# Optimization experiments

Hardware: AMD Instinct MI355X
Metric: run time of the kernel (lower is better)

## Reference

```python
import jax, jax.numpy as jnp
import numpy as np

B, N, K = 2, 8192, 9
FEAT_C, COST_C, FLOW_C = 128, 64, 3
CH = [128, 128]          # PointConv output channels
MLP = [128, 64]          # pointwise Conv1d channels
WN = 16                  # WeightNet output width
HID = [8, 8]             # WeightNet hidden widths
SLOPE = 0.1              # leaky relu slope
EPS = 1e-5
CLAMP = (-200.0, 200.0)


def setup_inputs() -> dict:
    key = jax.random.key(0)
    ks = iter(jax.random.split(key, 64))
    def nrm(shape, s=0.02):
        return jax.random.normal(next(ks), shape, jnp.float32) * s
    inp = {}
    inp["xyz"] = jax.random.normal(next(ks), (B, N, 3), jnp.float32)
    inp["feats"] = jax.random.normal(next(ks), (B, FEAT_C, N), jnp.float32)
    inp["cost_volume"] = jax.random.normal(next(ks), (B, COST_C, N), jnp.float32)
    inp["flow"] = jax.random.normal(next(ks), (B, FLOW_C, N), jnp.float32)
    last = FEAT_C + COST_C + FLOW_C
    for i, co in enumerate(CH):
        cin = last + 3
        p = f"pc{i}_"
        inp[p + "w1"] = nrm((HID[0], 3)); inp[p + "b1"] = jnp.zeros((HID[0],), jnp.float32)
        inp[p + "w2"] = nrm((HID[1], HID[0])); inp[p + "b2"] = jnp.zeros((HID[1],), jnp.float32)
        inp[p + "w3"] = nrm((WN, HID[1])); inp[p + "b3"] = jnp.zeros((WN,), jnp.float32)
        inp[p + "linW"] = nrm((co, cin * WN)); inp[p + "linb"] = jnp.zeros((co,), jnp.float32)
        last = co
    for i, co in enumerate(MLP):
        inp[f"mlp{i}_W"] = nrm((co, last)); inp[f"mlp{i}_b"] = jnp.zeros((co,), jnp.float32)
        last = co
    inp["fc_W"] = nrm((3, last)); inp["fc_b"] = jnp.zeros((3,), jnp.float32)
    return inp


def _bn(x, axes):
    m = x.mean(axes, keepdims=True)
    v = x.var(axes, keepdims=True)
    return (x - m) / jnp.sqrt(v + EPS)


def _leaky(x):
    return jnp.where(x >= 0, x, SLOPE * x)


def _knn_idx(xyz, k):
    # xyz: [B,N,3] -> idx [B,N,K] of k nearest (incl. self)
    sq = jnp.sum(xyz * xyz, -1)                       # [B,N]
    d = sq[:, :, None] + sq[:, None, :] - 2.0 * jnp.einsum('bnc,bmc->bnm', xyz, xyz)
    return jax.lax.top_k(-d, k)[1]                    # [B,N,K]


def _gather(a, idx):
    # a: [B,N,C], idx: [B,N,K] -> [B,N,K,C]
    return jax.vmap(lambda x, i: x[i])(a, idx)


def _pointconv(xyz, points, idx, w1, b1, w2, b2, w3, b3, linW, linb):
    # xyz [B,N,3], points [B,C,N] -> [B,out,N]
    g_xyz = _gather(xyz, idx) - xyz[:, :, None, :]    # [B,N,K,3] relative coords
    g_pts = _gather(jnp.transpose(points, (0, 2, 1)), idx)  # [B,N,K,C]
    grouped = jnp.concatenate([g_pts, g_xyz], -1)     # [B,N,K,C+3]
    # WeightNet on relative coords: 3 -> 8 -> 8 -> 16 (bn+relu each)
    h = jax.nn.relu(_bn(g_xyz @ w1.T + b1, (0, 1, 2)))
    h = jax.nn.relu(_bn(h @ w2.T + b2, (0, 1, 2)))
    w = jax.nn.relu(_bn(h @ w3.T + b3, (0, 1, 2)))    # [B,N,K,WN]
    bsz, n = grouped.shape[0], grouped.shape[1]
    agg = jnp.einsum('bnkc,bnkw->bncw', grouped, w).reshape(bsz, n, -1)
    out = agg @ linW.T + linb                         # [B,N,out]
    out = _leaky(_bn(out, (0, 1)))
    return jnp.transpose(out, (0, 2, 1))              # [B,out,N]


def reference(xyz, feats, cost_volume, flow,
              pc0_w1, pc0_b1, pc0_w2, pc0_b2, pc0_w3, pc0_b3, pc0_linW, pc0_linb,
              pc1_w1, pc1_b1, pc1_w2, pc1_b2, pc1_w3, pc1_b3, pc1_linW, pc1_linb,
              mlp0_W, mlp0_b, mlp1_W, mlp1_b, fc_W, fc_b):
    idx = _knn_idx(xyz, K)
    x = jnp.concatenate([feats, cost_volume, flow], axis=1)  # [B, feat+cost+flow, N]
    x = _pointconv(xyz, x, idx, pc0_w1, pc0_b1, pc0_w2, pc0_b2, pc0_w3, pc0_b3, pc0_linW, pc0_linb)
    x = _pointconv(xyz, x, idx, pc1_w1, pc1_b1, pc1_w2, pc1_b2, pc1_w3, pc1_b3, pc1_linW, pc1_linb)
    x = _leaky(jnp.einsum('oc,bcn->bon', mlp0_W, x) + mlp0_b[None, :, None])
    x = _leaky(jnp.einsum('oc,bcn->bon', mlp1_W, x) + mlp1_b[None, :, None])
    fl = jnp.einsum('oc,bcn->bon', fc_W, x) + fc_b[None, :, None]
    return x, jnp.clip(fl, CLAMP[0], CLAMP[1])
```

## Files before the change

kernel.cpp:

```cpp
#include <hip/hip_runtime.h>

#define NBATCH 2
#define NPTS   8192
#define NPT    (NBATCH*NPTS)
#define KNN    9
#define SEG    16
#define SEGN   (NPTS/SEG)
#define SCAP   16
#define SSTR   17

typedef unsigned short u16;
typedef unsigned int   u32;
typedef short bf16x8 __attribute__((ext_vector_type(8)));
typedef float f32x4  __attribute__((ext_vector_type(4)));

__device__ __forceinline__ float wred(float v){
#pragma unroll
  for(int o=32;o>0;o>>=1) v += __shfl_down(v,o);
  return v;
}

__device__ __forceinline__ u16 f2b(float f){
  u32 u = __float_as_uint(f);
  return (u16)((u + 0x7fffu + ((u>>16)&1u)) >> 16);
}

__device__ __forceinline__ float bumpup(float x){
  u32 u = __float_as_uint(x);
  if(u == 0x80000000u) u = 1u;
  else if((int)u >= 0) u += 1u;
  else u -= 1u;
  return __uint_as_float(u);
}

__global__ __launch_bounds__(256) void k_build_xin(
    const float* __restrict__ feats, const float* __restrict__ cost,
    const float* __restrict__ flow, float* __restrict__ xin)
{
  __shared__ float buf[196][67];
  int t = threadIdx.x;
  int pt0 = blockIdx.x*64;
  int b = pt0 >> 13, n0 = pt0 & (NPTS-1);
  int lane = t & 63, grp = t >> 6;
  const float* f  = feats + (size_t)b*128*NPTS + n0 + lane;
  const float* cv = cost  + (size_t)b*64 *NPTS + n0 + lane;
  const float* fl = flow  + (size_t)b*3  *NPTS + n0 + lane;
  for(int c=grp; c<128; c+=4) buf[c][lane]      = f[(size_t)c*NPTS];
  for(int c=grp; c<64;  c+=4) buf[128+c][lane]  = cv[(size_t)c*NPTS];
  if(grp<3) buf[192+grp][lane] = fl[(size_t)grp*NPTS];
  else      buf[195][lane] = 0.f;
  __syncthreads();
  for(int e=t; e<64*49; e+=256){
    int p = e/49, q = e-p*49;
    float4 v = make_float4(buf[4*q][p], buf[4*q+1][p], buf[4*q+2][p], buf[4*q+3][p]);
    *(float4*)(xin + (size_t)(pt0+p)*196 + 4*q) = v;
  }
}

__global__ __launch_bounds__(256) void k_thr(
    const float* __restrict__ xyz, float* __restrict__ thr)
{
  __shared__ float md[4][64][9];
  int t = threadIdx.x, lane = t & 63, wave = t >> 6;
  int qb = blockIdx.x;
  int b = qb >> 7;
  int n = (qb & 127)*64 + lane;
  const float* xb = xyz + (size_t)b*NPTS*3;
  float qx=xb[3*n], qy=xb[3*n+1], qz=xb[3*n+2];
  float qs = __fadd_rn(__fadd_rn(__fmul_rn(qx,qx),__fmul_rn(qy,qy)),__fmul_rn(qz,qz));
  float bd[KNN];
#pragma unroll
  for(int i=0;i<KNN;i++) bd[i]=__builtin_inff();
  for(int i=0;i<128;i++){
    int m = (wave*128 + i)*16;
    float cx=xb[3*m], cy=xb[3*m+1], cz=xb[3*m+2];
    float s = __fadd_rn(__fadd_rn(__fmul_rn(cx,cx),__fmul_rn(cy,cy)),__fmul_rn(cz,cz));
    float dot = fmaf(cz,qz, fmaf(cy,qy, __fmul_rn(cx,qx)));
    float d = __fsub_rn(__fadd_rn(qs,s), __fmul_rn(2.0f,dot));
    if(d < bd[KNN-1]){
      bd[KNN-1]=d;
#pragma unroll
      for(int r=KNN-2;r>=0;r--){
        if(bd[r+1] < bd[r]){ float td=bd[r]; bd[r]=bd[r+1]; bd[r+1]=td; }
      }
    }
  }
#pragma unroll
  for(int i=0;i<KNN;i++) md[wave][lane][i]=bd[i];
  __syncthreads();
  if(t < 64){
    float b2[KNN];
#pragma unroll
    for(int i=0;i<KNN;i++) b2[i]=__builtin_inff();
    for(int w=0;w<4;w++){
#pragma unroll
      for(int i=0;i<KNN;i++){
        float d = md[w][t][i];
        if(d < b2[KNN-1]){
          b2[KNN-1]=d;
#pragma unroll
          for(int r=KNN-2;r>=0;r--){
            if(b2[r+1] < b2[r]){ float td=b2[r]; b2[r]=b2[r+1]; b2[r+1]=td; }
          }
        }
      }
    }
    thr[(b<<13) + (qb & 127)*64 + t] = b2[KNN-1];
  }
}

__global__ __launch_bounds__(256) void k_knn_part(
    const float* __restrict__ xyz, const float* __restrict__ thr,
    float* __restrict__ pd, int* __restrict__ pi)
{
  __shared__ float4 cbuf[256];
  __shared__ float sdq[256*SSTR];
  __shared__ int   sqi[256*SSTR];
  int t = threadIdx.x;
  int seg = blockIdx.x & (SEG-1);
  int qc  = blockIdx.x >> 4;
  int b = qc >> 5;
  int n = (qc & 31)*256 + t;
  int pt = (b<<13) + n;
  const float* xb = xyz + (size_t)b*NPTS*3;
  float qx=xb[3*n], qy=xb[3*n+1], qz=xb[3*n+2];
  float qs = __fadd_rn(__fadd_rn(__fmul_rn(qx,qx),__fmul_rn(qy,qy)),__fmul_rn(qz,qz));
  float init = bumpup(thr[pt]);
  float bd[KNN]; int bi[KNN];
#pragma unroll
  for(int i=0;i<KNN;i++){ bd[i]=init; bi[i]=0x7fffffff; }
  float cut = init;
  int cnt = 0;
  float* msd = sdq + t*SSTR;
  int*   msi = sqi + t*SSTR;
  auto flush = [&](){
    for(int i=0;i<cnt;i++){
      float d = msd[i]; int id = msi[i];
      if(d < bd[KNN-1]){
        bd[KNN-1]=d; bi[KNN-1]=id;
#pragma unroll
        for(int r=KNN-2;r>=0;r--){
          if(bd[r+1] < bd[r]){
            float td=bd[r]; bd[r]=bd[r+1]; bd[r+1]=td;
            int ti=bi[r]; bi[r]=bi[r+1]; bi[r+1]=ti;
          }
        }
      }
    }
    cnt = 0;
    cut = bd[KNN-1];
  };
  const int m0 = seg*SEGN;
  for(int tt=0; tt<SEGN; tt+=256){
    int m = m0 + tt + t;
    float cx=xb[3*m], cy=xb[3*m+1], cz=xb[3*m+2];
    float s = __fadd_rn(__fadd_rn(__fmul_rn(cx,cx),__fmul_rn(cy,cy)),__fmul_rn(cz,cz));
    cbuf[t] = make_float4(cx,cy,cz,s);
    __syncthreads();
    for(int j0=0; j0<256; j0+=8){
      float dv[8];
#pragma unroll
      for(int u=0;u<8;u++){
        float4 c = cbuf[j0+u];
        float dot = fmaf(c.z,qz, fmaf(c.y,qy, __fmul_rn(c.x,qx)));
        dv[u] = __fsub_rn(__fadd_rn(qs,c.w), __fmul_rn(2.0f,dot));
      }
#pragma unroll
      for(int u=0;u<8;u++){
        if(dv[u] < cut){
          msd[cnt]=dv[u]; msi[cnt]=m0+tt+j0+u; cnt++;
          if(cnt==SCAP) flush();
        }
      }
    }
    __syncthreads();
  }
  flush();
  size_t base = ((size_t)pt*SEG + seg)*KNN;
#pragma unroll
  for(int i=0;i<KNN;i++){ pd[base+i]=bd[i]; pi[base+i]=bi[i]; }
}

__global__ __launch_bounds__(256) void k_knn_merge(
    const float* __restrict__ pd, const int* __restrict__ pi, int* __restrict__ idxo)
{
  int pt = blockIdx.x*256 + threadIdx.x;
  const float4* dp = (const float4*)(pd + (size_t)pt*SEG*KNN);
  const int4*   ip = (const int4*)(pi + (size_t)pt*SEG*KNN);
  float bd[KNN]; int bi[KNN];
#pragma unroll
  for(int i=0;i<KNN;i++){ bd[i]=__builtin_inff(); bi[i]=0x7fffffff; }
  for(int v=0; v<SEG*KNN/4; v++){
    float4 dv = dp[v];
    int4   iv = ip[v];
    float dd[4] = {dv.x,dv.y,dv.z,dv.w};
    int   ii[4] = {iv.x,iv.y,iv.z,iv.w};
#pragma unroll
    for(int u=0;u<4;u++){
      float d = dd[u]; int id = ii[u];
      if(d < bd[KNN-1]){
        bd[KNN-1]=d; bi[KNN-1]=id;
#pragma unroll
        for(int i=KNN-2;i>=0;i--){
          if(bd[i+1] < bd[i]){
            float td=bd[i]; bd[i]=bd[i+1]; bd[i+1]=td;
            int ti=bi[i]; bi[i]=bi[i+1]; bi[i+1]=ti;
          }
        }
      }
    }
  }
#pragma unroll
  for(int r=0;r<KNN;r++) idxo[pt*KNN + r] = bi[r];
}

__global__ __launch_bounds__(256) void k_wn1(
    const float* __restrict__ xyz, const int* __restrict__ idx,
    const float* __restrict__ W, const float* __restrict__ Bv,
    float* __restrict__ hout, float* __restrict__ partial)
{
  int t = threadIdx.x;
  int e = blockIdx.x*256 + t;
  int pt = e/KNN;
  int b = pt>>13, n = pt & (NPTS-1);
  int m = idx[e];
  const float* xb = xyz + (size_t)b*NPTS*3;
  float gx = xb[3*m]-xb[3*n], gy = xb[3*m+1]-xb[3*n+1], gz = xb[3*m+2]-xb[3*n+2];
  float v[8];
#pragma unroll
  for(int j=0;j<8;j++){
    float d = fmaf(gz, W[3*j+2], fmaf(gy, W[3*j+1], gx*W[3*j]));
    v[j] = d + Bv[j];
    hout[(size_t)e*8 + j] = v[j];
  }
  __shared__ float red[4][2][8];
  int wave = t>>6, lane = t&63;
#pragma unroll
  for(int j=0;j<8;j++){
    float s = wred(v[j]);
    float q = wred(v[j]*v[j]);
    if(lane==0){ red[wave][0][j]=s; red[wave][1][j]=q; }
  }
  __syncthreads();
  if(t < 16){
    int isq = t>>3, c = t&7;
    partial[blockIdx.x*16 + t] =
      red[0][isq][c]+red[1][isq][c]+red[2][isq][c]+red[3][isq][c];
  }
}

template<int CI, int CO>
__global__ __launch_bounds__(256) void k_wn23(
    const float* __restrict__ hin, const float* __restrict__ partialIn,
    int nb, float cnt,
    const float* __restrict__ W, const float* __restrict__ Bv,
    float* __restrict__ hout, float* __restrict__ partialOut)
{
  __shared__ float sa[256], qa[256];
  __shared__ float stl[2*CI];
  int t = threadIdx.x;
  {
    int c = t % CI;
    int r0 = t / CI;
    int stride = 256 / CI;
    float s=0.f, q=0.f;
    for(int r=r0; r<nb; r+=stride){
      s += partialIn[r*2*CI + c];
      q += partialIn[r*2*CI + CI + c];
    }
    sa[t]=s; qa[t]=q;
    __syncthreads();
    if(t < CI){
      for(int g=1; g<stride; g++){ s += sa[t+g*CI]; q += qa[t+g*CI]; }
      float mean = s/cnt;
      float var  = q/cnt - mean*mean;
      stl[t]    = mean;
      stl[CI+t] = 1.0f/sqrtf(var + 1e-5f);
    }
    __syncthreads();
  }
  int e = blockIdx.x*256 + t;
  float x[CI];
#pragma unroll
  for(int i=0;i<CI;i++){
    float v = (hin[(size_t)e*CI + i] - stl[i])*stl[CI+i];
    x[i] = v>0.f? v : 0.f;
  }
  float v[CO];
#pragma unroll
  for(int j=0;j<CO;j++){
    float d = 0.f;
#pragma unroll
    for(int i=0;i<CI;i++) d = fmaf(x[i], W[j*CI+i], d);
    v[j] = d + Bv[j];
    hout[(size_t)e*CO + j] = v[j];
  }
  __shared__ float red[4][2][CO];
  int wave = t>>6, lane = t&63;
#pragma unroll
  for(int j=0;j<CO;j++){
    float s = wred(v[j]);
    float q = wred(v[j]*v[j]);
    if(lane==0){ red[wave][0][j]=s; red[wave][1][j]=q; }
  }
  __syncthreads();
  if(t < 2*CO){
    int isq = t/CO, c = t%CO;
    partialOut[blockIdx.x*2*CO + t] =
      red[0][isq][c]+red[1][isq][c]+red[2][isq][c]+red[3][isq][c];
  }
}

__global__ __launch_bounds__(256) void k_fin(
    const float* __restrict__ partial, float* __restrict__ st,
    int C, int nb, float cnt)
{
  __shared__ float sa[256], qa[256];
  int t = threadIdx.x;
  int c = t % C;
  int r0 = t / C;
  int stride = 256 / C;
  float s=0.f, q=0.f;
  for(int r=r0; r<nb; r+=stride){
    s += partial[r*2*C + c];
    q += partial[r*2*C + C + c];
  }
  sa[t]=s; qa[t]=q;
  __syncthreads();
  if(t < C){
    for(int g=1; g<stride; g++){ s += sa[t+g*C]; q += qa[t+g*C]; }
    float mean = s/cnt;
    float var  = q/cnt - mean*mean;
    st[t]   = mean;
    st[C+t] = 1.0f/sqrtf(var + 1e-5f);
  }
}

__global__ __launch_bounds__(256) void k_prepW(
    const float* __restrict__ linW, u16* __restrict__ Wh, int AW, int KP)
{
  int e = blockIdx.x*256 + threadIdx.x;
  if(e >= 128*KP) return;
  int o = e / KP, k = e - o*KP;
  float w = (k < AW) ? linW[o*AW + k] : 0.f;
  Wh[e] = f2b(w);
}

template<int CIN, int XSTRIDE, int KP>
__global__ __launch_bounds__(256) void k_buildA(
    const float* __restrict__ xin, const float* __restrict__ xyz,
    const int* __restrict__ idx, const float* __restrict__ wpre,
    const float* __restrict__ st3, u16* __restrict__ Abuf, int c0)
{
  constexpr int P = 16;
  constexpr int CPTS = CIN-3;
  constexpr int CPAD = KP/16;
  __shared__ float wm[P][KNN][16];
  __shared__ float gxs[P][KNN][3];
  __shared__ int   si[P][KNN];
  __shared__ float sm3[16], sr3[16];
  int t = threadIdx.x;
  int pt0 = c0 + blockIdx.x*P;
  int b = pt0 >> 13;
  const float* xb = xyz + (size_t)b*NPTS*3;
  if(t<16){ sm3[t]=st3[t]; sr3[t]=st3[16+t]; }
  for(int e=t; e<P*KNN; e+=256){
    int p = e/KNN, k = e - p*KNN;
    int n = (pt0+p)&(NPTS-1);
    int m = idx[(pt0+p)*KNN+k];
    si[p][k]=m;
    gxs[p][k][0]=xb[3*m]  -xb[3*n];
    gxs[p][k][1]=xb[3*m+1]-xb[3*n+1];
    gxs[p][k][2]=xb[3*m+2]-xb[3*n+2];
  }
  __syncthreads();
  for(int e=t; e<P*KNN*16; e+=256){
    int p = e/(KNN*16); int r = e - p*(KNN*16); int k = r>>4, wn = r&15;
    float v = (wpre[((size_t)(pt0+p)*KNN + k)*16 + wn] - sm3[wn]) * sr3[wn];
    wm[p][k][wn] = v>0.f? v:0.f;
  }
  __syncthreads();
  for(int it=t; it<P*CPAD; it+=256){
    int p = it/CPAD, c = it - p*CPAD;
    u32 u[8];
    if(c < CIN){
      float g[KNN];
      if(c < CPTS){
#pragma unroll
        for(int k=0;k<KNN;k++)
          g[k] = xin[(size_t)((b<<13) + si[p][k])*XSTRIDE + c];
      } else {
        int cc = c - CPTS;
#pragma unroll
        for(int k=0;k<KNN;k++) g[k] = gxs[p][k][cc];
      }
      float a[16];
#pragma unroll
      for(int wn=0; wn<16; wn++){
        float s = 0.f;
#pragma unroll
        for(int k=0;k<KNN;k++) s = fmaf(g[k], wm[p][k][wn], s);
        a[wn] = s;
      }
#pragma unroll
      for(int j=0;j<8;j++)
        u[j] = (u32)f2b(a[2*j]) | ((u32)f2b(a[2*j+1])<<16);
    } else {
#pragma unroll
      for(int j=0;j<8;j++) u[j]=0;
    }
    u32* dst = (u32*)(Abuf + ((size_t)(blockIdx.x*P + p)*KP + c*16));
    uint4 v0 = make_uint4(u[0],u[1],u[2],u[3]);
    uint4 v1 = make_uint4(u[4],u[5],u[6],u[7]);
    *(uint4*)dst = v0;
    *((uint4*)dst + 1) = v1;
  }
}

__device__ __forceinline__ void gload16(const void* g, void* l){
  __builtin_amdgcn_global_load_lds(
      (const __attribute__((address_space(1))) u32*)g,
      (__attribute__((address_space(3))) u32*)l, 16, 0, 0);
}

template<int KP>
__global__ __launch_bounds__(512) void k_gemm(
    const u16* __restrict__ Wh, const u16* __restrict__ A,
    const float* __restrict__ linb, float* __restrict__ outp,
    float* __restrict__ partial, int ptBase)
{
  __shared__ __attribute__((aligned(16))) u16 lds[24576];
  constexpr int NT = KP/64;
  int t = threadIdx.x, wave = t>>6, lane = t&63;
  int p0 = blockIdx.x*64;
  const u16* Ab = A + (size_t)p0*KP;

  auto stage = [&](const u16* __restrict__ g, int k0, int ldsByteOff, int rows){
    int nr = (rows*128) >> 13;
    for(int r=0;r<nr;r++){
      int y  = (r*8 + wave) << 10;
      int yl = y + lane*16;
      int row = yl >> 7;
      int s = (yl >> 4) & 7;
      int c = s ^ (row & 7);
      const u16* src = g + (size_t)row*KP + k0 + c*8;
      gload16(src, (char*)lds + ldsByteOff + y);
    }
  };

  stage(Wh, 0, 0,     128);
  stage(Ab, 0, 32768, 64);

  f32x4 acc[4];
#pragma unroll
  for(int j=0;j<4;j++) acc[j]=(f32x4)(0.f);

  for(int kt=0; kt<NT; kt++){
    int cur = kt & 1;
    __syncthreads();
    if(kt+1 < NT){
      int nxt = cur^1;
      stage(Wh, (kt+1)*64, nxt*16384,         128);
      stage(Ab, (kt+1)*64, 32768 + nxt*8192,  64);
    }
    const u16* Lw = lds + cur*8192;
    const u16* La = lds + 16384 + cur*4096;
#pragma unroll
    for(int kf=0; kf<2; kf++){
      int cb = kf*4 + (lane>>4);
      bf16x8 af[4];
#pragma unroll
      for(int nf=0; nf<4; nf++){
        int p = nf*16 + (lane&15);
        af[nf] = *(const bf16x8*)(La + p*64 + ((cb ^ (p&7))<<3));
      }
      int row = wave*16 + (lane&15);
      bf16x8 wh = *(const bf16x8*)(Lw + row*64 + ((cb ^ (row&7))<<3));
#pragma unroll
      for(int nf=0; nf<4; nf++)
        acc[nf] = __builtin_amdgcn_mfma_f32_16x16x32_bf16(wh, af[nf], acc[nf], 0,0,0);
    }
  }

  int gb = (ptBase>>6) + blockIdx.x;
  int q = lane>>4, lc = lane&15;
  int obase = wave*16 + q*4;
#pragma unroll
  for(int r=0;r<4;r++){
    int o = obase + r;
    float bo = linb[o];
    float sv = 0.f, qv = 0.f;
#pragma unroll
    for(int nf=0; nf<4; nf++){
      float x = acc[nf][r] + bo;
      outp[(size_t)(ptBase + p0 + nf*16 + lc)*128 + o] = x;
      sv += x; qv = fmaf(x,x,qv);
    }
#pragma unroll
    for(int off=8; off>0; off>>=1){
      sv += __shfl_down(sv,off);
      qv += __shfl_down(qv,off);
    }
    if(lc==0){
      partial[gb*256 + o]       = sv;
      partial[gb*256 + 128 + o] = qv;
    }
  }
}

__global__ __launch_bounds__(256) void k_pfin(
    const float* __restrict__ outp, const float* __restrict__ st,
    float* __restrict__ xout)
{
  int e = blockIdx.x*256 + threadIdx.x;
  int c = e & 127;
  float v = (outp[e]-st[c])*st[128+c];
  xout[e] = v>=0.f? v : 0.1f*v;
}

__global__ __launch_bounds__(512) void k_mlp(
    const float* __restrict__ x2,
    const float* __restrict__ W0, const float* __restrict__ B0,
    const float* __restrict__ W1, const float* __restrict__ B1,
    const float* __restrict__ Wf, const float* __restrict__ Bf,
    float* __restrict__ dout)
{
  __shared__ float w0l[128*129];
  __shared__ float w1l[128*65];
  __shared__ float xt [128*65];
  __shared__ float m1l[64*65];
  int t = threadIdx.x;
  int pt0 = blockIdx.x*64;
  int b = pt0 >> 13, n0 = pt0 & (NPTS-1);
  for(int e=t; e<128*128; e+=512){ int o=e>>7, j=e&127; w0l[j*129+o] = W0[e]; }
  for(int e=t; e<64*128;  e+=512){ int o=e>>7, j=e&127; w1l[j*65+o]  = W1[e]; }
  for(int e=t; e<64*128;  e+=512){ int p=e>>7, j=e&127; xt[j*65+p]   = x2[(size_t)(pt0+p)*128 + j]; }
  __syncthreads();
  int p = t&63, wv = t>>6;
  float acc[16];
#pragma unroll
  for(int i=0;i<16;i++) acc[i]=0.f;
  for(int j=0;j<128;j++){
    float xv = xt[j*65+p];
#pragma unroll
    for(int i=0;i<16;i++)
      acc[i] = fmaf(w0l[j*129 + wv*16 + i], xv, acc[i]);
  }
  __syncthreads();
#pragma unroll
  for(int i=0;i<16;i++){
    int o = wv*16+i;
    float v = acc[i] + B0[o];
    v = v>=0.f? v : 0.1f*v;
    xt[o*65 + p] = v;
  }
  __syncthreads();
  float a2[8];
#pragma unroll
  for(int i=0;i<8;i++) a2[i]=0.f;
  for(int j=0;j<128;j++){
    float xv = xt[j*65+p];
#pragma unroll
    for(int i=0;i<8;i++)
      a2[i] = fmaf(w1l[j*65 + wv*8 + i], xv, a2[i]);
  }
#pragma unroll
  for(int i=0;i<8;i++){
    int o = wv*8+i;
    float v = a2[i] + B1[o];
    v = v>=0.f? v : 0.1f*v;
    dout[(size_t)(b*64+o)*NPTS + n0 + p] = v;
    m1l[o*65+p] = v;
  }
  __syncthreads();
  if(t < 192){
    int o = t/64, pp = t%64;
    float a = Bf[o];
    for(int j=0;j<64;j++) a = fmaf(Wf[o*64+j], m1l[j*65+pp], a);
    a = fminf(fmaxf(a, -200.f), 200.f);
    dout[(size_t)NBATCH*64*NPTS + (size_t)(b*3+o)*NPTS + n0 + pp] = a;
  }
}

extern "C" void kernel_launch(void* const* d_in, const int* in_sizes, int n_in,
                              void* d_out, int out_size, void* d_ws, size_t ws_size,
                              hipStream_t stream)
{
  (void)in_sizes; (void)n_in; (void)out_size;
  const float* xyz   = (const float*)d_in[0];
  const float* feats = (const float*)d_in[1];
  const float* cost  = (const float*)d_in[2];
  const float* flow  = (const float*)d_in[3];
  const float* pw1[2]  = {(const float*)d_in[4],  (const float*)d_in[12]};
  const float* pb1[2]  = {(const float*)d_in[5],  (const float*)d_in[13]};
  const float* pw2[2]  = {(const float*)d_in[6],  (const float*)d_in[14]};
  const float* pb2[2]  = {(const float*)d_in[7],  (const float*)d_in[15]};
  const float* pw3[2]  = {(const float*)d_in[8],  (const float*)d_in[16]};
  const float* pb3[2]  = {(const float*)d_in[9],  (const float*)d_in[17]};
  const float* plW[2]  = {(const float*)d_in[10], (const float*)d_in[18]};
  const float* plb[2]  = {(const float*)d_in[11], (const float*)d_in[19]};
  const float* m0W = (const float*)d_in[20];
  const float* m0b = (const float*)d_in[21];
  const float* m1W = (const float*)d_in[22];
  const float* m1b = (const float*)d_in[23];
  const float* fcW = (const float*)d_in[24];
  const float* fcb = (const float*)d_in[25];
  float* out = (float*)d_out;

  const int KP0 = 3200, AW0 = 3168;
  const int KP1 = 2112, AW1 = 2096;

  float* ws = (float*)d_ws;
  size_t o = 0;
  float* xin0 = ws + o; o += (size_t)NPT*196;
  int*   idx  = (int*)(ws + o); o += (size_t)NPT*KNN + 3;
  o &= ~(size_t)3;
  float* thr  = ws + o; o += (size_t)NPT;
  float* pd   = ws + o; o += (size_t)NPT*SEG*KNN;
  int*   pi   = (int*)(ws + o); o += (size_t)NPT*SEG*KNN;
  float* h1   = ws + o; o += (size_t)NPT*KNN*8;
  float* h2   = ws + o; o += (size_t)NPT*KNN*8;
  float* wpre = ws + o; o += (size_t)NPT*KNN*16;
  float* part1 = ws + o; o += 576*16;
  float* part2 = ws + o; o += 576*16;
  float* part3 = ws + o; o += 576*32;
  float* parto = ws + o; o += 65536;
  float* st3  = ws + o; o += 32;
  float* sto  = ws + o; o += 256;
  float* outp = ws + o; o += (size_t)NPT*128;
  float* x1   = ws + o; o += (size_t)NPT*128;
  float* x2   = ws + o; o += (size_t)NPT*128;
  u16* Wh0 = (u16*)(ws + o); o += (size_t)128*KP0/2;
  u16* Wh1 = (u16*)(ws + o); o += (size_t)128*KP1/2;
  u16* Abuf = (u16*)(ws + o);
  size_t used_bytes = o*4;
  size_t avail = ws_size > used_bytes ? ws_size - used_bytes : 0;
  int npc = NPT;
  while(npc > 1024 && (size_t)npc*KP0*2 > avail) npc >>= 1;

  k_build_xin<<<NPT/64, 256, 0, stream>>>(feats, cost, flow, xin0);
  k_thr<<<256, 256, 0, stream>>>(xyz, thr);
  k_knn_part<<<64*SEG, 256, 0, stream>>>(xyz, thr, pd, pi);
  k_knn_merge<<<NPT/256, 256, 0, stream>>>(pd, pi, idx);

  k_prepW<<<(128*KP0+255)/256, 256, 0, stream>>>(plW[0], Wh0, AW0, KP0);
  k_prepW<<<(128*KP1+255)/256, 256, 0, stream>>>(plW[1], Wh1, AW1, KP1);

  const float cnt1 = (float)(NPT*KNN);
  const float cnto = (float)NPT;

  for(int L=0; L<2; ++L){
    k_wn1<<<576,256,0,stream>>>(xyz, idx, pw1[L], pb1[L], h1, part1);
    k_wn23<8,8><<<576,256,0,stream>>>(h1, part1, 576, cnt1, pw2[L], pb2[L], h2, part2);
    k_wn23<8,16><<<576,256,0,stream>>>(h2, part2, 576, cnt1, pw3[L], pb3[L], wpre, part3);
    k_fin<<<1,256,0,stream>>>(part3, st3, 16, 576, cnt1);
    for(int c0 = 0; c0 < NPT; c0 += npc){
      if(L==0){
        k_buildA<198,196,KP0><<<npc/16,256,0,stream>>>(xin0, xyz, idx, wpre, st3, Abuf, c0);
        k_gemm<KP0><<<npc/64,512,0,stream>>>(Wh0, Abuf, plb[0], outp, parto, c0);
      } else {
        k_buildA<131,128,KP1><<<npc/16,256,0,stream>>>(x1, xyz, idx, wpre, st3, Abuf, c0);
        k_gemm<KP1><<<npc/64,512,0,stream>>>(Wh1, Abuf, plb[1], outp, parto, c0);
      }
    }
    k_fin<<<1,256,0,stream>>>(parto, sto, 128, NPT/64, cnto);
    k_pfin<<<NPT*128/256,256,0,stream>>>(outp, sto, (L==0)? x1 : x2);
  }

  k_mlp<<<NPT/64,512,0,stream>>>(x2, m0W,m0b, m1W,m1b, fcW,fcb, out);
}
```

Before: 561.2 us.

## Fuse BN/leaky epilogues into consumers, derive WeightNet layer-1 stats from xyz moments

Removes the k_pfin pass by applying the PointConv batch-norm and leaky ReLU inside the next buildA gather and inside k_mlp's load. WeightNet layer-1 BN statistics are now computed analytically from first and second moments of neighbour offsets, accumulated once in k_knn_merge, so the k_wn1 kernel and its h1 buffer are dropped and layer 1 is fused into the layer-2 kernel. The knn candidate insertion becomes branchless, always writing to the scratch slot and flushing when more than 8 are pending. Costs are repeated BN work on gathered neighbours (9x redundant) and a small serial reduction at the start of every wn23a block.

New measurement: 566.4 us. No clear change (+0.9%).

```diff
diff --git a/kernel.cpp b/kernel.cpp
--- a/kernel.cpp
+++ b/kernel.cpp
@@ -121,7 +121,8 @@
   int qc  = blockIdx.x >> 4;
   int b = qc >> 5;
   int n = (qc & 31)*256 + t;
-  int pt = (b<<13) + n;
+  int pt = (b<<13) + t + (qc&31)*256;
+  pt = (b<<13) + n;
   const float* xb = xyz + (size_t)b*NPTS*3;
   float qx=xb[3*n], qy=xb[3*n+1], qz=xb[3*n+2];
   float qs = __fadd_rn(__fadd_rn(__fmul_rn(qx,qx),__fmul_rn(qy,qy)),__fmul_rn(qz,qz));
@@ -167,11 +168,11 @@
       }
 #pragma unroll
       for(int u=0;u<8;u++){
-        if(dv[u] < cut){
-          msd[cnt]=dv[u]; msi[cnt]=m0+tt+j0+u; cnt++;
-          if(cnt==SCAP) flush();
-        }
-      }
+        msd[cnt] = dv[u];
+        msi[cnt] = m0+tt+j0+u;
+        cnt += (dv[u] < cut) ? 1 : 0;
+      }
+      if(cnt > 8) flush();
     }
     __syncthreads();
   }
@@ -182,9 +183,15 @@
 }
 
 __global__ __launch_bounds__(256) void k_knn_merge(
-    const float* __restrict__ pd, const int* __restrict__ pi, int* __restrict__ idxo)
-{
-  int pt = blockIdx.x*256 + threadIdx.x;
+    const float* __restrict__ xyz,
+    const float* __restrict__ pd, const int* __restrict__ pi,
+    int* __restrict__ idxo, float* __restrict__ gpart)
+{
+  __shared__ float red[4][9];
+  int t = threadIdx.x;
+  int pt = blockIdx.x*256 + t;
+  int b = pt >> 13, n = pt & (NPTS-1);
+  const float* xb = xyz + (size_t)b*NPTS*3;
   const float4* dp = (const float4*)(pd + (size_t)pt*SEG*KNN);
   const int4*   ip = (const int4*)(pi + (size_t)pt*SEG*KNN);
   float bd[KNN]; int bi[KNN];
@@ -212,25 +219,82 @@
   }
 #pragma unroll
   for(int r=0;r<KNN;r++) idxo[pt*KNN + r] = bi[r];
-}
-
-__global__ __launch_bounds__(256) void k_wn1(
+  float q0=xb[3*n], q1=xb[3*n+1], q2=xb[3*n+2];
+  float mom[9];
+#pragma unroll
+  for(int i=0;i<9;i++) mom[i]=0.f;
+#pragma unroll
+  for(int r=0;r<KNN;r++){
+    int m = bi[r];
+    float gx=xb[3*m]-q0, gy=xb[3*m+1]-q1, gz=xb[3*m+2]-q2;
+    mom[0]+=gx; mom[1]+=gy; mom[2]+=gz;
+    mom[3]=fmaf(gx,gx,mom[3]); mom[4]=fmaf(gy,gy,mom[4]); mom[5]=fmaf(gz,gz,mom[5]);
+    mom[6]=fmaf(gx,gy,mom[6]); mom[7]=fmaf(gx,gz,mom[7]); mom[8]=fmaf(gy,gz,mom[8]);
+  }
+  int wave = t>>6, lane = t&63;
+#pragma unroll
+  for(int i=0;i<9;i++){
+    float s = wred(mom[i]);
+    if(lane==0) red[wave][i]=s;
+  }
+  __syncthreads();
+  if(t<9)
+    gpart[blockIdx.x*9 + t] = red[0][t]+red[1][t]+red[2][t]+red[3][t];
+}
+
+__global__ __launch_bounds__(256) void k_wn23a(
     const float* __restrict__ xyz, const int* __restrict__ idx,
-    const float* __restrict__ W, const float* __restrict__ Bv,
-    float* __restrict__ hout, float* __restrict__ partial)
-{
+    const float* __restrict__ gpart, float cnt,
+    const float* __restrict__ W1, const float* __restrict__ B1,
+    const float* __restrict__ W2, const float* __restrict__ B2,
+    float* __restrict__ hout, float* __restrict__ partialOut)
+{
+  __shared__ float mom[9];
+  __shared__ float stl[16];
   int t = threadIdx.x;
+  if(t<9){
+    float s=0.f;
+    for(int r=0;r<64;r++) s += gpart[r*9+t];
+    mom[t]=s;
+  }
+  __syncthreads();
+  if(t<8){
+    float inv = 1.0f/cnt;
+    float w0=W1[3*t], w1=W1[3*t+1], w2=W1[3*t+2], bb=B1[t];
+    float Eg0=mom[0]*inv, Eg1=mom[1]*inv, Eg2=mom[2]*inv;
+    float Mxx=mom[3]*inv, Myy=mom[4]*inv, Mzz=mom[5]*inv;
+    float Mxy=mom[6]*inv, Mxz=mom[7]*inv, Myz=mom[8]*inv;
+    float mu_lin = w0*Eg0 + w1*Eg1 + w2*Eg2;
+    float mean = mu_lin + bb;
+    float e2 = w0*w0*Mxx + w1*w1*Myy + w2*w2*Mzz
+             + 2.f*(w0*w1*Mxy + w0*w2*Mxz + w1*w2*Myz)
+             + 2.f*bb*mu_lin + bb*bb;
+    float var = e2 - mean*mean;
+    stl[t] = mean;
+    stl[8+t] = 1.0f/sqrtf(var + 1e-5f);
+  }
+  __syncthreads();
   int e = blockIdx.x*256 + t;
   int pt = e/KNN;
   int b = pt>>13, n = pt & (NPTS-1);
   int m = idx[e];
   const float* xb = xyz + (size_t)b*NPTS*3;
   float gx = xb[3*m]-xb[3*n], gy = xb[3*m+1]-xb[3*n+1], gz = xb[3*m+2]-xb[3*n+2];
+  float x[8];
+#pragma unroll
+  for(int j=0;j<8;j++){
+    float d = fmaf(gz, W1[3*j+2], fmaf(gy, W1[3*j+1], gx*W1[3*j]));
+    float v = d + B1[j];
+    v = (v - stl[j])*stl[8+j];
+    x[j] = v>0.f? v : 0.f;
+  }
   float v[8];
 #pragma unroll
   for(int j=0;j<8;j++){
-    float d = fmaf(gz, W[3*j+2], fmaf(gy, W[3*j+1], gx*W[3*j]));
-    v[j] = d + Bv[j];
+    float d = 0.f;
+#pragma unroll
+    for(int i=0;i<8;i++) d = fmaf(x[i], W2[j*8+i], d);
+    v[j] = d + B2[j];
     hout[(size_t)e*8 + j] = v[j];
   }
   __shared__ float red[4][2][8];
@@ -244,7 +308,7 @@
   __syncthreads();
   if(t < 16){
     int isq = t>>3, c = t&7;
-    partial[blockIdx.x*16 + t] =
+    partialOut[blockIdx.x*16 + t] =
       red[0][isq][c]+red[1][isq][c]+red[2][isq][c]+red[3][isq][c];
   }
 }
@@ -346,11 +410,12 @@
   Wh[e] = f2b(w);
 }
 
-template<int CIN, int XSTRIDE, int KP>
+template<int CIN, int XSTRIDE, int KP, bool BN>
 __global__ __launch_bounds__(256) void k_buildA(
     const float* __restrict__ xin, const float* __restrict__ xyz,
     const int* __restrict__ idx, const float* __restrict__ wpre,
-    const float* __restrict__ st3, u16* __restrict__ Abuf, int c0)
+    const float* __restrict__ st3, const float* __restrict__ bnst,
+    u16* __restrict__ Abuf, int c0)
 {
   constexpr int P = 16;
   constexpr int CPTS = CIN-3;
@@ -389,6 +454,14 @@
 #pragma unroll
         for(int k=0;k<KNN;k++)
           g[k] = xin[(size_t)((b<<13) + si[p][k])*XSTRIDE + c];
+        if(BN){
+          float sm = bnst[c], sr = bnst[128+c];
+#pragma unroll
+          for(int k=0;k<KNN;k++){
+            float v = (g[k]-sm)*sr;
+            g[k] = v>=0.f? v : 0.1f*v;
+          }
+        }
       } else {
         int cc = c - CPTS;
 #pragma unroll
@@ -410,10 +483,8 @@
       for(int j=0;j<8;j++) u[j]=0;
     }
     u32* dst = (u32*)(Abuf + ((size_t)(blockIdx.x*P + p)*KP + c*16));
-    uint4 v0 = make_uint4(u[0],u[1],u[2],u[3]);
-    uint4 v1 = make_uint4(u[4],u[5],u[6],u[7]);
-    *(uint4*)dst = v0;
-    *((uint4*)dst + 1) = v1;
+    *(uint4*)dst       = make_uint4(u[0],u[1],u[2],u[3]);
+    *((uint4*)dst + 1) = make_uint4(u[4],u[5],u[6],u[7]);
   }
 }
 
@@ -508,18 +579,8 @@
   }
 }
 
-__global__ __launch_bounds__(256) void k_pfin(
-    const float* __restrict__ outp, const float* __restrict__ st,
-    float* __restrict__ xout)
-{
-  int e = blockIdx.x*256 + threadIdx.x;
-  int c = e & 127;
-  float v = (outp[e]-st[c])*st[128+c];
-  xout[e] = v>=0.f? v : 0.1f*v;
-}
-
 __global__ __launch_bounds__(512) void k_mlp(
-    const float* __restrict__ x2,
+    const float* __restrict__ outp1, const float* __restrict__ sto,
     const float* __restrict__ W0, const float* __restrict__ B0,
     const float* __restrict__ W1, const float* __restrict__ B1,
     const float* __restrict__ Wf, const float* __restrict__ Bf,
@@ -534,7 +595,12 @@
   int b = pt0 >> 13, n0 = pt0 & (NPTS-1);
   for(int e=t; e<128*128; e+=512){ int o=e>>7, j=e&127; w0l[j*129+o] = W0[e]; }
   for(int e=t; e<64*128;  e+=512){ int o=e>>7, j=e&127; w1l[j*65+o]  = W1[e]; }
-  for(int e=t; e<64*128;  e+=512){ int p=e>>7, j=e&127; xt[j*65+p]   = x2[(size_t)(pt0+p)*128 + j]; }
+  for(int e=t; e<64*128;  e+=512){
+    int p=e>>7, j=e&127;
+    float v = outp1[(size_t)(pt0+p)*128 + j];
+    v = (v - sto[j])*sto[128+j];
+    xt[j*65+p] = v>=0.f? v : 0.1f*v;
+  }
   __syncthreads();
   int p = t&63, wv = t>>6;
   float acc[16];
@@ -618,18 +684,17 @@
   float* thr  = ws + o; o += (size_t)NPT;
   float* pd   = ws + o; o += (size_t)NPT*SEG*KNN;
   int*   pi   = (int*)(ws + o); o += (size_t)NPT*SEG*KNN;
-  float* h1   = ws + o; o += (size_t)NPT*KNN*8;
   float* h2   = ws + o; o += (size_t)NPT*KNN*8;
   float* wpre = ws + o; o += (size_t)NPT*KNN*16;
-  float* part1 = ws + o; o += 576*16;
+  float* gpart = ws + o; o += 64*9 + 7;
   float* part2 = ws + o; o += 576*16;
   float* part3 = ws + o; o += 576*32;
   float* parto = ws + o; o += 65536;
   float* st3  = ws + o; o += 32;
-  float* sto  = ws + o; o += 256;
-  float* outp = ws + o; o += (size_t)NPT*128;
-  float* x1   = ws + o; o += (size_t)NPT*128;
-  float* x2   = ws + o; o += (size_t)NPT*128;
+  float* sto0 = ws + o; o += 256;
+  float* sto1 = ws + o; o += 256;
+  float* outp0 = ws + o; o += (size_t)NPT*128;
+  float* outp1 = ws + o; o += (size_t)NPT*128;
   u16* Wh0 = (u16*)(ws + o); o += (size_t)128*KP0/2;
   u16* Wh1 = (u16*)(ws + o); o += (size_t)128*KP1/2;
   u16* Abuf = (u16*)(ws + o);
@@ -641,7 +706,7 @@
   k_build_xin<<<NPT/64, 256, 0, stream>>>(feats, cost, flow, xin0);
   k_thr<<<256, 256, 0, stream>>>(xyz, thr);
   k_knn_part<<<64*SEG, 256, 0, stream>>>(xyz, thr, pd, pi);
-  k_knn_merge<<<NPT/256, 256, 0, stream>>>(pd, pi, idx);
+  k_knn_merge<<<NPT/256, 256, 0, stream>>>(xyz, pd, pi, idx, gpart);
 
   k_prepW<<<(128*KP0+255)/256, 256, 0, stream>>>(plW[0], Wh0, AW0, KP0);
   k_prepW<<<(128*KP1+255)/256, 256, 0, stream>>>(plW[1], Wh1, AW1, KP1);
@@ -650,22 +715,21 @@
   const float cnto = (float)NPT;
 
   for(int L=0; L<2; ++L){
-    k_wn1<<<576,256,0,stream>>>(xyz, idx, pw1[L], pb1[L], h1, part1);
-    k_wn23<8,8><<<576,256,0,stream>>>(h1, part1, 576, cnt1, pw2[L], pb2[L], h2, part2);
+    k_wn23a<<<576,256,0,stream>>>(xyz, idx, gpart, cnt1,
+                                  pw1[L], pb1[L], pw2[L], pb2[L], h2, part2);
     k_wn23<8,16><<<576,256,0,stream>>>(h2, part2, 576, cnt1, pw3[L], pb3[L], wpre, part3);
     k_fin<<<1,256,0,stream>>>(part3, st3, 16, 576, cnt1);
     for(int c0 = 0; c0 < NPT; c0 += npc){
       if(L==0){
-        k_buildA<198,196,KP0><<<npc/16,256,0,stream>>>(xin0, xyz, idx, wpre, st3, Abuf, c0);
-        k_gemm<KP0><<<npc/64,512,0,stream>>>(Wh0, Abuf, plb[0], outp, parto, c0);
+        k_buildA<198,196,KP0,false><<<npc/16,256,0,stream>>>(xin0, xyz, idx, wpre, st3, sto0, Abuf, c0);
+        k_gemm<KP0><<<npc/64,512,0,stream>>>(Wh0, Abuf, plb[0], outp0, parto, c0);
       } else {
-        k_buildA<131,128,KP1><<<npc/16,256,0,stream>>>(x1, xyz, idx, wpre, st3, Abuf, c0);
-        k_gemm<KP1><<<npc/64,512,0,stream>>>(Wh1, Abuf, plb[1], outp, parto, c0);
-      }
-    }
-    k_fin<<<1,256,0,stream>>>(parto, sto, 128, NPT/64, cnto);
-    k_pfin<<<NPT*128/256,256,0,stream>>>(outp, sto, (L==0)? x1 : x2);
-  }
-
-  k_mlp<<<NPT/64,512,0,stream>>>(x2, m0W,m0b, m1W,m1b, fcW,fcb, out);
-}
+        k_buildA<131,128,KP1,true><<<npc/16,256,0,stream>>>(outp0, xyz, idx, wpre, st3, sto0, Abuf, c0);
+        k_gemm<KP1><<<npc/64,512,0,stream>>>(Wh1, Abuf, plb[1], outp1, parto, c0);
+      }
+    }
+    k_fin<<<1,256,0,stream>>>(parto, (L==0)? sto0 : sto1, 128, NPT/64, cnto);
+  }
+
+  k_mlp<<<NPT/64,512,0,stream>>>(outp1, sto1, m0W,m0b, m1W,m1b, fcW,fcb, out);
+}
```
